# Performance work log

Hardware: AMD Instinct MI355X
Metric: run time of the kernel (lower is better)

## Reference

```python
import jax, jax.numpy as jnp
import numpy as np

C_LOGIT = 10.0  # logit range hyperparameter (use_tanh=True)


def setup_inputs() -> dict:
    key = jax.random.key(0)
    ks = jax.random.split(key, 7)
    B, S, D = 64, 2048, 512
    s = 1.0 / np.sqrt(D)
    return {
        "query": jax.random.normal(ks[0], (B, D), jnp.float32),
        "ref": jax.random.normal(ks[1], (B, S, D), jnp.float32),
        "Wq_w": jax.random.uniform(ks[2], (D, D), jnp.float32, -s, s),
        "Wq_b": jax.random.uniform(ks[3], (D,), jnp.float32, -s, s),
        "Wr_w": jax.random.uniform(ks[4], (D, D), jnp.float32, -s, s),  # Conv1d k=1 == Linear
        "Wr_b": jax.random.uniform(ks[5], (D,), jnp.float32, -s, s),
        "value": jax.random.uniform(ks[6], (D,), jnp.float32, -s, s),
    }


def reference(query, ref, Wq_w, Wq_b, Wr_w, Wr_b, value):
    # query: [B, D], ref: [B, S, D]
    q = query @ Wq_w.T + Wq_b                                  # [B, D]  (Wq linear)
    r = jnp.einsum("bsd,ed->bse", ref, Wr_w) + Wr_b            # [B, S, D] (Conv1d k=1 over permuted ref)
    h = jnp.tanh(q[:, None, :] + r)                            # broadcast query over seq_len
    logits = jnp.einsum("bsd,d->bs", h, value)                 # <v, tanh(Wq q + Wr r)>
    logits = C_LOGIT * jnp.tanh(logits)                        # use_tanh=True
    ref_out = jnp.transpose(r, (0, 2, 1))                      # [B, D, S] as returned by torch branch
    return ref_out, logits
```

## Files before the change

kernel.cpp:

```cpp
#include <hip/hip_runtime.h>
#include <stdint.h>

#define NB  64
#define SEQ 2048
#define DIM 512
#define NS  (NB*SEQ)

typedef __bf16 bf16x8 __attribute__((ext_vector_type(8)));
typedef float  f32x4  __attribute__((ext_vector_type(4)));
typedef unsigned int u32;
typedef unsigned short u16;
typedef unsigned int u32x4 __attribute__((ext_vector_type(4)));

__device__ __forceinline__ u32 pk_bf16(float a, float b){
  union {float f; u32 i;} x, y; x.f = a; y.f = b;
  return ((x.i + 0x8000u) >> 16) | ((y.i + 0x8000u) & 0xffff0000u);
}
__device__ __forceinline__ float fast_tanh(float x){
  float e = __builtin_amdgcn_exp2f(x * 2.885390081777927f);
  return 1.0f - 2.0f*__builtin_amdgcn_rcpf(e + 1.0f);
}

__global__ void wconv_kernel(const float* __restrict__ Wr_w, u16* __restrict__ wrbf)
{
  const int i = blockIdx.x*256 + threadIdx.x;
  const int eb = i >> 10, kt = (i >> 6) & 15, quad = (i >> 4) & 3, col = i & 15;
  const float* g = Wr_w + (size_t)(eb*16 + col)*DIM + kt*32 + quad*8;
  f32x4 a = *(const f32x4*)g, c = *(const f32x4*)(g + 4);
  u32x4 p;
  p[0]=pk_bf16(a.x,a.y); p[1]=pk_bf16(a.z,a.w);
  p[2]=pk_bf16(c.x,c.y); p[3]=pk_bf16(c.z,c.w);
  ((u32x4*)wrbf)[i] = p;
}

__global__ void q_kernel(const float* __restrict__ query, const float* __restrict__ Wq_w,
                         const float* __restrict__ Wq_b, float* __restrict__ qws)
{
  __shared__ float lq[DIM];
  const int b   = blockIdx.x;
  const int tid = threadIdx.x;
  const int e   = blockIdx.y*256 + tid;
  for (int i = tid; i < DIM; i += 256) lq[i] = query[b*DIM + i];
  __syncthreads();
  const float* wr = Wq_w + (size_t)e*DIM;
  float acc = 0.f;
  for (int d = 0; d < DIM; d += 4){
    f32x4 w = *(const f32x4*)(wr + d);
    acc += w.x*lq[d] + w.y*lq[d+1] + w.z*lq[d+2] + w.w*lq[d+3];
  }
  qws[b*DIM + e] = acc + Wq_b[e];
}

#define BN 64

__global__ __launch_bounds__(256, 2)
void main_kernel(const float* __restrict__ ref,  const u16* __restrict__ wrbf,
                 const float* __restrict__ Wr_b, const float* __restrict__ value,
                 const float* __restrict__ qws,  float* __restrict__ out)
{
  __shared__ __align__(16) char smem[66560];
  char*  refL = smem;
  float* lred = (float*)(smem + 65536);

  const int tid  = threadIdx.x;
  const int lane = tid & 63, wave = tid >> 6;
  const int col  = lane & 15, quad = lane >> 4;
  const size_t s0 = (size_t)blockIdx.x * BN;
  const int b  = (int)(s0 >> 11);
  const int sb = (int)(s0 & 2047);

  auto wptr = [&](int K, int f){
    const int eh = K >> 4, kt = K & 15;
    const int eb = eh*16 + (f>>1)*8 + wave*2 + (f&1);
    return (const bf16x8*)(wrbf + ((size_t)((eb*16 + kt)*64 + lane))*8);
  };

  bf16x8 wb[4][4];
#pragma unroll
  for (int f = 0; f < 4; ++f) wb[0][f] = *wptr(0, f);

  float bb[8], qq[8], vv[8];
#pragma unroll
  for (int i = 0; i < 8; ++i){
    const int e = (i>>2)*256 + ((i>>1)&1)*128 + wave*32 + (i&1)*16 + col;
    bb[i] = Wr_b[e]; qq[i] = qws[b*DIM + e]; vv[i] = value[e];
  }

#pragma unroll 4
  for (int it = 0; it < 16; ++it){
    const int c   = it*256 + tid;
    const int row = c >> 6, ch = c & 63;
    const float* g = ref + (s0 + row)*DIM + ch*8;
    f32x4 x0 = *(const f32x4*)g, x1 = *(const f32x4*)(g+4);
    u32x4 p;
    p[0]=pk_bf16(x0.x,x0.y); p[1]=pk_bf16(x0.z,x0.w);
    p[2]=pk_bf16(x1.x,x1.y); p[3]=pk_bf16(x1.z,x1.w);
    *(u32x4*)(refL + row*1024 + (ch ^ (row&7))*16) = p;
  }
#pragma unroll
  for (int f = 0; f < 4; ++f) wb[1][f] = *wptr(1, f);
  __syncthreads();

  f32x4 acc[2][2][4];
#pragma unroll
  for (int et = 0; et < 2; ++et)
#pragma unroll
    for (int mi = 0; mi < 2; ++mi)
#pragma unroll
      for (int ni = 0; ni < 4; ++ni) acc[et][mi][ni] = (f32x4)0.0f;
  float ls[4][4];
#pragma unroll
  for (int ni = 0; ni < 4; ++ni)
#pragma unroll
    for (int rg = 0; rg < 4; ++rg) ls[ni][rg] = 0.f;

  bf16x8 rbuf[2][4];
#pragma unroll
  for (int ni = 0; ni < 4; ++ni){
    const int r = ni*16 + col;
    rbuf[0][ni] = *(const bf16x8*)(refL + r*1024 + ((quad ^ (r&7)))*16);
  }

#pragma unroll
  for (int eh = 0; eh < 2; ++eh){
#pragma unroll
    for (int kt = 0; kt < 16; ++kt){
      const int K = eh*16 + kt;
      if (K + 2 < 32){
#pragma unroll
        for (int f = 0; f < 4; ++f) wb[(K+2)&3][f] = *wptr(K+2, f);
      }
      if (K + 1 < 32){
        const int nk = (K+1) & 15;
#pragma unroll
        for (int ni = 0; ni < 4; ++ni){
          const int r = ni*16 + col;
          rbuf[(K+1)&1][ni] = *(const bf16x8*)(refL + r*1024 + (((nk*4 + quad) ^ (r&7)))*16);
        }
      }
#pragma unroll
      for (int f = 0; f < 4; ++f)
#pragma unroll
        for (int ni = 0; ni < 4; ++ni)
          acc[f>>1][f&1][ni] = __builtin_amdgcn_mfma_f32_16x16x32_bf16(
              rbuf[K&1][ni], wb[K&3][f], acc[f>>1][f&1][ni], 0, 0, 0);
    }

#pragma unroll
    for (int et = 0; et < 2; ++et)
#pragma unroll
      for (int mi = 0; mi < 2; ++mi){
        const int i = eh*4 + et*2 + mi;
        const int e = eh*256 + et*128 + wave*32 + mi*16 + col;
        float* orow = out + ((size_t)(b*DIM + e))*SEQ + sb + quad*4;
#pragma unroll
        for (int ni = 0; ni < 4; ++ni){
          f32x4 v = acc[et][mi][ni];
          v.x += bb[i]; v.y += bb[i]; v.z += bb[i]; v.w += bb[i];
          *(f32x4*)(orow + ni*16) = v;
          ls[ni][0] += fast_tanh(qq[i] + v.x) * vv[i];
          ls[ni][1] += fast_tanh(qq[i] + v.y) * vv[i];
          ls[ni][2] += fast_tanh(qq[i] + v.z) * vv[i];
          ls[ni][3] += fast_tanh(qq[i] + v.w) * vv[i];
          if (eh == 0) acc[et][mi][ni] = (f32x4)0.0f;
        }
      }
  }

#pragma unroll
  for (int ni = 0; ni < 4; ++ni)
#pragma unroll
    for (int rg = 0; rg < 4; ++rg){
      float x = ls[ni][rg];
      x += __shfl_xor(x, 1); x += __shfl_xor(x, 2);
      x += __shfl_xor(x, 4); x += __shfl_xor(x, 8);
      ls[ni][rg] = x;
    }
  if (col == 0){
#pragma unroll
    for (int ni = 0; ni < 4; ++ni)
#pragma unroll
      for (int rg = 0; rg < 4; ++rg)
        lred[wave*64 + ni*16 + quad*4 + rg] = ls[ni][rg];
  }
  __syncthreads();
  if (tid < BN){
    const float s = lred[tid] + lred[64+tid] + lred[128+tid] + lred[192+tid];
    out[(size_t)NB*DIM*SEQ + b*SEQ + sb + tid] = 10.0f * fast_tanh(s);
  }
}

extern "C" void kernel_launch(void* const* d_in, const int* in_sizes, int n_in,
                              void* d_out, int out_size, void* d_ws, size_t ws_size,
                              hipStream_t stream)
{
  const float* query = (const float*)d_in[0];
  const float* ref   = (const float*)d_in[1];
  const float* Wq_w  = (const float*)d_in[2];
  const float* Wq_b  = (const float*)d_in[3];
  const float* Wr_w  = (const float*)d_in[4];
  const float* Wr_b  = (const float*)d_in[5];
  const float* value = (const float*)d_in[6];
  float* out = (float*)d_out;

  float* qws  = (float*)d_ws;
  u16*   wrbf = (u16*)((float*)d_ws + NB*DIM);

  wconv_kernel<<<dim3(128), dim3(256), 0, stream>>>(Wr_w, wrbf);
  q_kernel<<<dim3(NB, 2), dim3(256), 0, stream>>>(query, Wq_w, Wq_b, qws);
  main_kernel<<<dim3(NS/BN), dim3(256), 0, stream>>>(ref, wrbf, Wr_b, value, qws, out);
}
```

Before: 522.4 us.

## Make main kernel persistent with double-buffered LDS prefetch of ref tiles

Replaces the one-tile-per-block launch with 256 blocks of 512 threads, each processing 8 consecutive 64-row tiles. The next tile's fp32 ref rows are loaded into registers, converted to bf16 and written into a second 64KB LDS buffer while the current tile's MFMAs run. This hides global load latency behind compute and removes the per-block prologue. Each wave now owns 64 output channels across the full K, so the output is produced in one pass instead of two halves. The cost is 132KB of LDS per block, which limits residency, plus higher register pressure from the staging registers.

```diff
diff --git a/kernel.cpp b/kernel.cpp
--- a/kernel.cpp
+++ b/kernel.cpp
@@ -51,142 +51,180 @@
   qws[b*DIM + e] = acc + Wq_b[e];
 }
 
-#define BN 64
-
-__global__ __launch_bounds__(256, 2)
+__global__ __launch_bounds__(512, 2)
 void main_kernel(const float* __restrict__ ref,  const u16* __restrict__ wrbf,
                  const float* __restrict__ Wr_b, const float* __restrict__ value,
                  const float* __restrict__ qws,  float* __restrict__ out)
 {
-  __shared__ __align__(16) char smem[66560];
-  char*  refL = smem;
-  float* lred = (float*)(smem + 65536);
+  __shared__ __align__(16) char smem[135168];
+  float* lred = (float*)(smem + 131072);
 
   const int tid  = threadIdx.x;
   const int lane = tid & 63, wave = tid >> 6;
   const int col  = lane & 15, quad = lane >> 4;
-  const size_t s0 = (size_t)blockIdx.x * BN;
-  const int b  = (int)(s0 >> 11);
-  const int sb = (int)(s0 & 2047);
-
-  auto wptr = [&](int K, int f){
-    const int eh = K >> 4, kt = K & 15;
-    const int eb = eh*16 + (f>>1)*8 + wave*2 + (f&1);
-    return (const bf16x8*)(wrbf + ((size_t)((eb*16 + kt)*64 + lane))*8);
+
+  const int t0 = blockIdx.x * 8;
+  const int b  = t0 >> 5;
+
+  float bb[4], qq[4], vv[4];
+#pragma unroll
+  for (int mi = 0; mi < 4; ++mi){
+    const int e = wave*64 + mi*16 + col;
+    bb[mi] = Wr_b[e]; qq[mi] = qws[b*DIM + e]; vv[mi] = value[e];
+  }
+
+  auto wptr = [&](int kt, int mi){
+    return (const bf16x8*)(wrbf + ((size_t)((wave*4 + mi)*1024 + kt*64 + lane))*8);
   };
 
-  bf16x8 wb[4][4];
-#pragma unroll
-  for (int f = 0; f < 4; ++f) wb[0][f] = *wptr(0, f);
-
-  float bb[8], qq[8], vv[8];
-#pragma unroll
-  for (int i = 0; i < 8; ++i){
-    const int e = (i>>2)*256 + ((i>>1)&1)*128 + wave*32 + (i&1)*16 + col;
-    bb[i] = Wr_b[e]; qq[i] = qws[b*DIM + e]; vv[i] = value[e];
-  }
-
-#pragma unroll 4
-  for (int it = 0; it < 16; ++it){
-    const int c   = it*256 + tid;
-    const int row = c >> 6, ch = c & 63;
-    const float* g = ref + (s0 + row)*DIM + ch*8;
-    f32x4 x0 = *(const f32x4*)g, x1 = *(const f32x4*)(g+4);
-    u32x4 p;
-    p[0]=pk_bf16(x0.x,x0.y); p[1]=pk_bf16(x0.z,x0.w);
-    p[2]=pk_bf16(x1.x,x1.y); p[3]=pk_bf16(x1.z,x1.w);
-    *(u32x4*)(refL + row*1024 + (ch ^ (row&7))*16) = p;
-  }
-#pragma unroll
-  for (int f = 0; f < 4; ++f) wb[1][f] = *wptr(1, f);
+  {
+    const float* src = ref + ((size_t)t0*64 + wave)*DIM + lane*8;
+#pragma unroll
+    for (int j = 0; j < 8; ++j){
+      const float* g = src + (size_t)j*8*DIM;
+      f32x4 x0 = *(const f32x4*)g, x1 = *(const f32x4*)(g+4);
+      u32x4 p;
+      p[0]=pk_bf16(x0.x,x0.y); p[1]=pk_bf16(x0.z,x0.w);
+      p[2]=pk_bf16(x1.x,x1.y); p[3]=pk_bf16(x1.z,x1.w);
+      *(u32x4*)(smem + (j*8+wave)*1024 + (lane^wave)*16) = p;
+    }
+  }
+  bf16x8 wb[2][4];
+#pragma unroll
+  for (int mi = 0; mi < 4; ++mi) wb[0][mi] = *wptr(0, mi);
   __syncthreads();
-
-  f32x4 acc[2][2][4];
-#pragma unroll
-  for (int et = 0; et < 2; ++et)
-#pragma unroll
-    for (int mi = 0; mi < 2; ++mi)
-#pragma unroll
-      for (int ni = 0; ni < 4; ++ni) acc[et][mi][ni] = (f32x4)0.0f;
-  float ls[4][4];
-#pragma unroll
-  for (int ni = 0; ni < 4; ++ni)
-#pragma unroll
-    for (int rg = 0; rg < 4; ++rg) ls[ni][rg] = 0.f;
 
   bf16x8 rbuf[2][4];
 #pragma unroll
   for (int ni = 0; ni < 4; ++ni){
     const int r = ni*16 + col;
-    rbuf[0][ni] = *(const bf16x8*)(refL + r*1024 + ((quad ^ (r&7)))*16);
-  }
-
-#pragma unroll
-  for (int eh = 0; eh < 2; ++eh){
+    rbuf[0][ni] = *(const bf16x8*)(smem + r*1024 + ((quad ^ (col&7)))*16);
+  }
+
+  f32x4 sx[4][2];
+
+#pragma unroll 1
+  for (int i = 0; i < 8; ++i){
+    char* curL = smem + ((i & 1) << 16);
+    char* nxtL = smem + (((i & 1) ^ 1) << 16);
+    const bool st = (i < 7);
+    const int sb = ((t0 + i) & 31) * 64;
+    const float* nsrc = ref + ((size_t)(t0+i+1)*64 + wave)*DIM + lane*8;
+
+    f32x4 acc[4][4];
+#pragma unroll
+    for (int mi = 0; mi < 4; ++mi)
+#pragma unroll
+      for (int ni = 0; ni < 4; ++ni) acc[mi][ni] = (f32x4)0.0f;
+    float ls[4][4];
+#pragma unroll
+    for (int ni = 0; ni < 4; ++ni)
+#pragma unroll
+      for (int rg = 0; rg < 4; ++rg) ls[ni][rg] = 0.f;
+
 #pragma unroll
     for (int kt = 0; kt < 16; ++kt){
-      const int K = eh*16 + kt;
-      if (K + 2 < 32){
-#pragma unroll
-        for (int f = 0; f < 4; ++f) wb[(K+2)&3][f] = *wptr(K+2, f);
-      }
-      if (K + 1 < 32){
-        const int nk = (K+1) & 15;
+#pragma unroll
+      for (int mi = 0; mi < 4; ++mi) wb[(kt+1)&1][mi] = *wptr((kt+1)&15, mi);
+
+      if (st && kt == 0){
+#pragma unroll
+        for (int j = 0; j < 4; ++j){
+          const float* g = nsrc + (size_t)j*8*DIM;
+          sx[j][0] = *(const f32x4*)g; sx[j][1] = *(const f32x4*)(g+4);
+        }
+      }
+      if (st && (kt == 4 || kt == 5)){
+#pragma unroll
+        for (int jj = 0; jj < 2; ++jj){
+          const int j = (kt-4)*2 + jj;
+          u32x4 p;
+          p[0]=pk_bf16(sx[j][0].x,sx[j][0].y); p[1]=pk_bf16(sx[j][0].z,sx[j][0].w);
+          p[2]=pk_bf16(sx[j][1].x,sx[j][1].y); p[3]=pk_bf16(sx[j][1].z,sx[j][1].w);
+          *(u32x4*)(nxtL + (j*8+wave)*1024 + (lane^wave)*16) = p;
+        }
+      }
+      if (st && kt == 8){
+#pragma unroll
+        for (int j = 0; j < 4; ++j){
+          const float* g = nsrc + (size_t)(j+4)*8*DIM;
+          sx[j][0] = *(const f32x4*)g; sx[j][1] = *(const f32x4*)(g+4);
+        }
+      }
+      if (st && (kt == 12 || kt == 13)){
+#pragma unroll
+        for (int jj = 0; jj < 2; ++jj){
+          const int j = (kt-12)*2 + jj;
+          u32x4 p;
+          p[0]=pk_bf16(sx[j][0].x,sx[j][0].y); p[1]=pk_bf16(sx[j][0].z,sx[j][0].w);
+          p[2]=pk_bf16(sx[j][1].x,sx[j][1].y); p[3]=pk_bf16(sx[j][1].z,sx[j][1].w);
+          *(u32x4*)(nxtL + ((j+4)*8+wave)*1024 + (lane^wave)*16) = p;
+        }
+      }
+
+      if (kt < 15){
 #pragma unroll
         for (int ni = 0; ni < 4; ++ni){
           const int r = ni*16 + col;
-          rbuf[(K+1)&1][ni] = *(const bf16x8*)(refL + r*1024 + (((nk*4 + quad) ^ (r&7)))*16);
-        }
-      }
-#pragma unroll
-      for (int f = 0; f < 4; ++f)
+          rbuf[(kt+1)&1][ni] = *(const bf16x8*)(curL + r*1024 + ((((kt+1)*4+quad) ^ (col&7)))*16);
+        }
+      }
+
+#pragma unroll
+      for (int mi = 0; mi < 4; ++mi)
 #pragma unroll
         for (int ni = 0; ni < 4; ++ni)
-          acc[f>>1][f&1][ni] = __builtin_amdgcn_mfma_f32_16x16x32_bf16(
-              rbuf[K&1][ni], wb[K&3][f], acc[f>>1][f&1][ni], 0, 0, 0);
-    }
-
-#pragma unroll
-    for (int et = 0; et < 2; ++et)
-#pragma unroll
-      for (int mi = 0; mi < 2; ++mi){
-        const int i = eh*4 + et*2 + mi;
-        const int e = eh*256 + et*128 + wave*32 + mi*16 + col;
-        float* orow = out + ((size_t)(b*DIM + e))*SEQ + sb + quad*4;
-#pragma unroll
-        for (int ni = 0; ni < 4; ++ni){
-          f32x4 v = acc[et][mi][ni];
-          v.x += bb[i]; v.y += bb[i]; v.z += bb[i]; v.w += bb[i];
-          *(f32x4*)(orow + ni*16) = v;
-          ls[ni][0] += fast_tanh(qq[i] + v.x) * vv[i];
-          ls[ni][1] += fast_tanh(qq[i] + v.y) * vv[i];
-          ls[ni][2] += fast_tanh(qq[i] + v.z) * vv[i];
-          ls[ni][3] += fast_tanh(qq[i] + v.w) * vv[i];
-          if (eh == 0) acc[et][mi][ni] = (f32x4)0.0f;
-        }
-      }
-  }
-
-#pragma unroll
-  for (int ni = 0; ni < 4; ++ni)
-#pragma unroll
-    for (int rg = 0; rg < 4; ++rg){
-      float x = ls[ni][rg];
-      x += __shfl_xor(x, 1); x += __shfl_xor(x, 2);
-      x += __shfl_xor(x, 4); x += __shfl_xor(x, 8);
-      ls[ni][rg] = x;
-    }
-  if (col == 0){
+          acc[mi][ni] = __builtin_amdgcn_mfma_f32_16x16x32_bf16(
+              rbuf[kt&1][ni], wb[kt&1][mi], acc[mi][ni], 0, 0, 0);
+    }
+
+#pragma unroll
+    for (int mi = 0; mi < 4; ++mi){
+      const int e = wave*64 + mi*16 + col;
+      float* orow = out + ((size_t)(b*DIM + e))*SEQ + sb + quad*4;
+#pragma unroll
+      for (int ni = 0; ni < 4; ++ni){
+        f32x4 v = acc[mi][ni];
+        v.x += bb[mi]; v.y += bb[mi]; v.z += bb[mi]; v.w += bb[mi];
+        *(f32x4*)(orow + ni*16) = v;
+        ls[ni][0] += fast_tanh(qq[mi] + v.x) * vv[mi];
+        ls[ni][1] += fast_tanh(qq[mi] + v.y) * vv[mi];
+        ls[ni][2] += fast_tanh(qq[mi] + v.z) * vv[mi];
+        ls[ni][3] += fast_tanh(qq[mi] + v.w) * vv[mi];
+      }
+    }
+
 #pragma unroll
     for (int ni = 0; ni < 4; ++ni)
 #pragma unroll
-      for (int rg = 0; rg < 4; ++rg)
-        lred[wave*64 + ni*16 + quad*4 + rg] = ls[ni][rg];
-  }
-  __syncthreads();
-  if (tid < BN){
-    const float s = lred[tid] + lred[64+tid] + lred[128+tid] + lred[192+tid];
-    out[(size_t)NB*DIM*SEQ + b*SEQ + sb + tid] = 10.0f * fast_tanh(s);
+      for (int rg = 0; rg < 4; ++rg){
+        float x = ls[ni][rg];
+        x += __shfl_xor(x, 1); x += __shfl_xor(x, 2);
+        x += __shfl_xor(x, 4); x += __shfl_xor(x, 8);
+        ls[ni][rg] = x;
+      }
+    float* lr = lred + (i & 1) * 512;
+    if (col == 0){
+#pragma unroll
+      for (int ni = 0; ni < 4; ++ni)
+#pragma unroll
+        for (int rg = 0; rg < 4; ++rg)
+          lr[wave*64 + ni*16 + quad*4 + rg] = ls[ni][rg];
+    }
+    __syncthreads();
+    if (tid < 64){
+      float s = 0.f;
+#pragma unroll
+      for (int w = 0; w < 8; ++w) s += lr[w*64 + tid];
+      out[(size_t)NB*DIM*SEQ + (size_t)b*SEQ + sb + tid] = 10.0f * fast_tanh(s);
+    }
+    if (st){
+#pragma unroll
+      for (int ni = 0; ni < 4; ++ni){
+        const int r = ni*16 + col;
+        rbuf[0][ni] = *(const bf16x8*)(nxtL + r*1024 + ((quad ^ (col&7)))*16);
+      }
+    }
   }
 }
 
@@ -208,5 +246,5 @@
 
   wconv_kernel<<<dim3(128), dim3(256), 0, stream>>>(Wr_w, wrbf);
   q_kernel<<<dim3(NB, 2), dim3(256), 0, stream>>>(query, Wq_w, Wq_b, qws);
-  main_kernel<<<dim3(NS/BN), dim3(256), 0, stream>>>(ref, wrbf, Wr_b, value, qws, out);
-}
+  main_kernel<<<dim3(256), dim3(512), 0, stream>>>(ref, wrbf, Wr_b, value, qws, out);
+}
```

Result: slower. 668.9 us (+28.0%).
